# Kernel optimization log

Hardware: AMD Instinct MI355X
Metric: run time of the kernel (lower is better)

The kernel has to match this reference:

```python
import jax, jax.numpy as jnp
import numpy as np

NUM_HEADS = 8
OUT_DIM = 128
DEPTH = OUT_DIM // NUM_HEADS  # 16


def setup_inputs() -> dict:
    key = jax.random.key(0)
    ks = jax.random.split(key, 6)
    B, N, F_IN = 32, 512, 64
    x = jax.random.normal(ks[0], (B, N, F_IN), dtype=jnp.float32)
    adj = jax.random.uniform(ks[1], (B, N, N), dtype=jnp.float32)
    wq = jax.random.normal(ks[2], (F_IN, OUT_DIM), dtype=jnp.float32) * 0.05
    wk = jax.random.normal(ks[3], (F_IN, OUT_DIM), dtype=jnp.float32) * 0.05
    wv = jax.random.normal(ks[4], (F_IN, OUT_DIM), dtype=jnp.float32) * 0.05
    wo = jax.random.normal(ks[5], (OUT_DIM, OUT_DIM), dtype=jnp.float32) * 0.05
    return {"x": x, "adj": adj, "wq": wq, "wk": wk, "wv": wv, "wo": wo}


def _split_heads(t, B, N):
    # [B, N, out_dim] -> [B, H, N, D]
    return t.reshape(B, N, NUM_HEADS, DEPTH).transpose(0, 2, 1, 3)


def reference(x, adj, wq, wk, wv, wo):
    B, N, _ = x.shape
    q = _split_heads(x @ wq, B, N)  # [B,H,N,D]
    k = _split_heads(x @ wk, B, N)
    v = _split_heads(x @ wv, B, N)
    scale = jnp.sqrt(jnp.float32(DEPTH))
    scores = jnp.einsum("bhnd,bhmd->bhnm", q, k) / scale  # [B,H,N,N]
    attn = jnp.tanh(scores * adj[:, None, :, :])  # mask-multiply + tanh
    h = jnp.einsum("bhnm,bhmd->bhnd", attn, v)  # [B,H,N,D]
    h = h.transpose(0, 2, 1, 3).reshape(B, N, OUT_DIM)
    return jax.nn.relu(h @ wo)
```

## Files before the change

kernel.cpp:

```cpp
#include <hip/hip_runtime.h>


typedef __bf16 bf16x8 __attribute__((ext_vector_type(8)));
typedef __bf16 bf16x4 __attribute__((ext_vector_type(4)));
typedef float  f32x4  __attribute__((ext_vector_type(4)));

#define MFMA16(a, b, c) __builtin_amdgcn_mfma_f32_16x16x32_bf16((a), (b), (c), 0, 0, 0)

__global__ __launch_bounds__(256) void prep_kernel(
    const float* __restrict__ wq, const float* __restrict__ wk,
    const float* __restrict__ wv, const float* __restrict__ wo,
    __bf16* __restrict__ WTb, __bf16* __restrict__ WoTb)
{
    int idx = blockIdx.x * 256 + threadIdx.x;
    if (idx < 6144) {
        int j4 = idx % 96, k = idx / 96, j = j4 * 4;
        const float* w = (j < 128) ? wq : ((j < 256) ? wk : wv);
        f32x4 v = *(const f32x4*)&w[k * 128 + (j & 127)];
#pragma unroll
        for (int e = 0; e < 4; ++e) WTb[(j + e) * 64 + k] = (__bf16)v[e];
    } else if (idx < 6144 + 4096) {
        int i2 = idx - 6144;
        int j4 = i2 % 32, k = i2 / 32, j = j4 * 4;
        f32x4 v = *(const f32x4*)&wo[k * 128 + j];
#pragma unroll
        for (int e = 0; e < 4; ++e) WoTb[(j + e) * 128 + k] = (__bf16)v[e];
    }
}

__global__ __launch_bounds__(256) void qkv_kernel(
    const float* __restrict__ x, const __bf16* __restrict__ WTb,
    __bf16* __restrict__ Qb, __bf16* __restrict__ Kb, __bf16* __restrict__ VT)
{
    const int tid = threadIdx.x, lane = tid & 63, w = tid >> 6;
    const int g = lane >> 4, lr = lane & 15;
    const long R0 = (long)blockIdx.x * 16;
    const int b = (int)(R0 >> 9);
    const int nloc = (int)(R0 & 511) + g * 4;

    bf16x8 af[2];
#pragma unroll
    for (int kk = 0; kk < 2; ++kk) {
        const float* xp = x + (R0 + lr) * 64 + kk * 32 + g * 8;
        f32x4 x0 = *(const f32x4*)xp, x1 = *(const f32x4*)(xp + 4);
        bf16x8 a;
#pragma unroll
        for (int e = 0; e < 4; ++e) { a[e] = (__bf16)x0[e]; a[4 + e] = (__bf16)x1[e]; }
        af[kk] = a;
    }

#pragma unroll 2
    for (int i = 0; i < 6; ++i) {
        const int j0 = (w * 6 + i) * 16;
        f32x4 acc = {0.f, 0.f, 0.f, 0.f};
#pragma unroll
        for (int kk = 0; kk < 2; ++kk) {
            bf16x8 bf = *(const bf16x8*)&WTb[(j0 + lr) * 64 + kk * 32 + g * 8];
            acc = MFMA16(af[kk], bf, acc);
        }
        const int jj = (j0 + lr) & 127, hh = jj >> 4, d = jj & 15;
        const int bh = b * 8 + hh, t = j0 >> 7;
        if (t == 2) {
            bf16x4 pk;
#pragma unroll
            for (int r = 0; r < 4; ++r) pk[r] = (__bf16)acc[r];
            *(bf16x4*)&VT[((long)bh * 16 + d) * 512 + nloc] = pk;
        } else {
            __bf16* dst = t ? Kb : Qb;
#pragma unroll
            for (int r = 0; r < 4; ++r)
                dst[((long)bh * 512 + nloc + r) * 16 + d] = (__bf16)acc[r];
        }
    }
}

__device__ __forceinline__ float tanh_e(float x) {
    float e = __builtin_amdgcn_exp2f(x);
    return 1.0f - 2.0f * __builtin_amdgcn_rcpf(e + 1.0f);
}

struct Tile {
    bf16x8 kf0, kf1;
    bf16x4 v0, v1;
};

__device__ __forceinline__ Tile load_tile(
    int m0, bool ga, const __bf16* Kbase, int lr, int g, const __bf16* Vrow)
{
    Tile t;
    t.kf0 = {}; t.kf1 = {};
    if (ga) {
        t.kf0 = *(const bf16x8*)&Kbase[(m0 + lr) * 16 + g * 8];
        t.kf1 = *(const bf16x8*)&Kbase[(m0 + 16 + lr) * 16 + g * 8];
    }
    t.v0 = *(const bf16x4*)&Vrow[m0 + g * 4];
    t.v1 = *(const bf16x4*)&Vrow[m0 + 16 + g * 4];
    return t;
}

__device__ __forceinline__ void compute_tile(
    const Tile& t, int m0, bf16x8 qf0, bf16x8 qf1,
    const __bf16* aR0, const __bf16* aR1, int g,
    f32x4& acc0, f32x4& acc1)
{
    bf16x4 ba00 = *(const bf16x4*)&aR0[m0 + g * 4];
    bf16x4 ba01 = *(const bf16x4*)&aR0[m0 + 16 + g * 4];
    bf16x4 ba10 = *(const bf16x4*)&aR1[m0 + g * 4];
    bf16x4 ba11 = *(const bf16x4*)&aR1[m0 + 16 + g * 4];

    const f32x4 z = {0.f, 0.f, 0.f, 0.f};
    f32x4 s00 = MFMA16(t.kf0, qf0, z);
    f32x4 s01 = MFMA16(t.kf1, qf0, z);
    f32x4 s10 = MFMA16(t.kf0, qf1, z);
    f32x4 s11 = MFMA16(t.kf1, qf1, z);

    bf16x8 p0, p1, vf;
#pragma unroll
    for (int r = 0; r < 4; ++r) {
        p0[r]     = (__bf16)tanh_e(s00[r] * (float)ba00[r]);
        p0[4 + r] = (__bf16)tanh_e(s01[r] * (float)ba01[r]);
        p1[r]     = (__bf16)tanh_e(s10[r] * (float)ba10[r]);
        p1[4 + r] = (__bf16)tanh_e(s11[r] * (float)ba11[r]);
        vf[r]     = t.v0[r];
        vf[4 + r] = t.v1[r];
    }
    acc0 = MFMA16(p0, vf, acc0);
    acc1 = MFMA16(p1, vf, acc1);
}

__global__ __launch_bounds__(512, 4) void attn_kernel(
    const float* __restrict__ adj,
    const __bf16* __restrict__ Qb, const __bf16* __restrict__ Kb,
    const __bf16* __restrict__ VT, const __bf16* __restrict__ WoTb,
    float* __restrict__ out)
{
    __shared__ __align__(16) char smem[33280];

    const int tid  = threadIdx.x;
    const int lane = tid & 63;
    const int h    = tid >> 6;
    const int g    = lane >> 4;
    const int lr   = lane & 15;

    const int l  = blockIdx.x;
    const int q  = l >> 3;
    const int b  = (q >> 4) * 8 + (l & 7);
    const int n0 = (q & 15) * 32;
    const int bh = b * 8 + h;

    const float C = 0.7213475204444817f;
    __bf16* adjL = (__bf16*)smem;
    const float* strip = adj + ((long)b * 512 + n0) * 512;
#pragma unroll
    for (int i = 0; i < 8; ++i) {
        int o = i * 2048 + tid * 4;
        f32x4 v = __builtin_nontemporal_load((const f32x4*)(strip + o));
        int row = o >> 9, col = o & 511;
        bf16x4 w;
#pragma unroll
        for (int e = 0; e < 4; ++e) w[e] = (__bf16)(v[e] * C);
        *(bf16x4*)&adjL[row * 520 + col] = w;
    }

    const bool ga = (g < 2);
    bf16x8 qf0 = {}, qf1 = {};
    if (ga) {
        qf0 = *(const bf16x8*)&Qb[((long)bh * 512 + n0 + lr) * 16 + g * 8];
        qf1 = *(const bf16x8*)&Qb[((long)bh * 512 + n0 + 16 + lr) * 16 + g * 8];
    }
    const __bf16* Kbase = Kb + (long)bh * 512 * 16;
    const __bf16* Vrow  = VT + ((long)bh * 16 + lr) * 512;
    const __bf16* aR0   = adjL + lr * 520;
    const __bf16* aR1   = adjL + (16 + lr) * 520;

    __syncthreads();

    f32x4 acc0 = {0.f, 0.f, 0.f, 0.f}, acc1 = {0.f, 0.f, 0.f, 0.f};

    Tile tA = load_tile(0, ga, Kbase, lr, g, Vrow);
#pragma unroll 1
    for (int t = 0; t < 16; t += 2) {
        Tile tB = load_tile((t + 1) * 32, ga, Kbase, lr, g, Vrow);
        compute_tile(tA, t * 32, qf0, qf1, aR0, aR1, g, acc0, acc1);
        if (t + 2 < 16)
            tA = load_tile((t + 2) * 32, ga, Kbase, lr, g, Vrow);
        compute_tile(tB, (t + 1) * 32, qf0, qf1, aR0, aR1, g, acc0, acc1);
    }

    __syncthreads();
    float* hL = (float*)smem;
#pragma unroll
    for (int r = 0; r < 4; ++r) {
        hL[(g * 4 + r) * 132 + h * 16 + lr]        = acc0[r];
        hL[(16 + g * 4 + r) * 132 + h * 16 + lr]   = acc1[r];
    }
    __syncthreads();

    f32x4 o0 = {0.f, 0.f, 0.f, 0.f}, o1 = {0.f, 0.f, 0.f, 0.f};
#pragma unroll
    for (int kt = 0; kt < 4; ++kt) {
        bf16x8 wf = *(const bf16x8*)&WoTb[(h * 16 + lr) * 128 + kt * 32 + g * 8];
        const float* hp0 = &hL[lr * 132 + kt * 32 + g * 8];
        const float* hp1 = &hL[(16 + lr) * 132 + kt * 32 + g * 8];
        f32x4 ha = *(const f32x4*)hp0, hb = *(const f32x4*)(hp0 + 4);
        f32x4 hc = *(const f32x4*)hp1, hd = *(const f32x4*)(hp1 + 4);
        bf16x8 a0, a1;
#pragma unroll
        for (int e = 0; e < 4; ++e) {
            a0[e] = (__bf16)ha[e]; a0[4 + e] = (__bf16)hb[e];
            a1[e] = (__bf16)hc[e]; a1[4 + e] = (__bf16)hd[e];
        }
        o0 = MFMA16(a0, wf, o0);
        o1 = MFMA16(a1, wf, o1);
    }

    const long obase = (long)b * 512 + n0;
#pragma unroll
    for (int r = 0; r < 4; ++r) {
        out[(obase + g * 4 + r) * 128 + h * 16 + lr]      = fmaxf(o0[r], 0.f);
        out[(obase + 16 + g * 4 + r) * 128 + h * 16 + lr] = fmaxf(o1[r], 0.f);
    }
}

extern "C" void kernel_launch(void* const* d_in, const int* in_sizes, int n_in,
                              void* d_out, int out_size, void* d_ws, size_t ws_size,
                              hipStream_t stream) {
    const float* x   = (const float*)d_in[0];
    const float* adj = (const float*)d_in[1];
    const float* wq  = (const float*)d_in[2];
    const float* wk  = (const float*)d_in[3];
    const float* wv  = (const float*)d_in[4];
    const float* wo  = (const float*)d_in[5];
    float* out = (float*)d_out;

    char* wsb = (char*)d_ws;
    __bf16* WTb  = (__bf16*)wsb;
    __bf16* WoTb = (__bf16*)(wsb + 49152);
    __bf16* Qb   = (__bf16*)(wsb + 81920);
    __bf16* Kb   = Qb + 2097152;
    __bf16* VT   = Kb + 2097152;

    prep_kernel<<<40, 256, 0, stream>>>(wq, wk, wv, wo, WTb, WoTb);
    qkv_kernel<<<1024, 256, 0, stream>>>(x, WTb, Qb, Kb, VT);
    attn_kernel<<<512, 512, 0, stream>>>(adj, Qb, Kb, VT, WoTb, out);
}
```

Baseline: 124.3 us.

## Deepen K/V prefetch to three tiles ahead and raise wave priority around MFMA

The attention inner loop now keeps three K/V tiles in flight instead of one, fully unrolled into a 4-tile rotating schedule with a drained epilogue. This hides more global load latency. It also wraps the compute section in s_setprio(1)/s_setprio(0) so waves doing MFMA/tanh work get issue priority over waves that are loading. The trade is higher register pressure under launch_bounds(512,4), which could cause spills or lower occupancy.

```diff
diff --git a/kernel.cpp b/kernel.cpp
--- a/kernel.cpp
+++ b/kernel.cpp
@@ -108,6 +108,7 @@
     bf16x4 ba10 = *(const bf16x4*)&aR1[m0 + g * 4];
     bf16x4 ba11 = *(const bf16x4*)&aR1[m0 + 16 + g * 4];
 
+    __builtin_amdgcn_s_setprio(1);
     const f32x4 z = {0.f, 0.f, 0.f, 0.f};
     f32x4 s00 = MFMA16(t.kf0, qf0, z);
     f32x4 s01 = MFMA16(t.kf1, qf0, z);
@@ -126,6 +127,7 @@
     }
     acc0 = MFMA16(p0, vf, acc0);
     acc1 = MFMA16(p1, vf, acc1);
+    __builtin_amdgcn_s_setprio(0);
 }
 
 __global__ __launch_bounds__(512, 4) void attn_kernel(
@@ -177,15 +179,27 @@
 
     f32x4 acc0 = {0.f, 0.f, 0.f, 0.f}, acc1 = {0.f, 0.f, 0.f, 0.f};
 
-    Tile tA = load_tile(0, ga, Kbase, lr, g, Vrow);
-#pragma unroll 1
-    for (int t = 0; t < 16; t += 2) {
-        Tile tB = load_tile((t + 1) * 32, ga, Kbase, lr, g, Vrow);
-        compute_tile(tA, t * 32, qf0, qf1, aR0, aR1, g, acc0, acc1);
-        if (t + 2 < 16)
-            tA = load_tile((t + 2) * 32, ga, Kbase, lr, g, Vrow);
-        compute_tile(tB, (t + 1) * 32, qf0, qf1, aR0, aR1, g, acc0, acc1);
-    }
+    Tile T0 = load_tile(0 * 32, ga, Kbase, lr, g, Vrow);
+    Tile T1 = load_tile(1 * 32, ga, Kbase, lr, g, Vrow);
+    Tile T2 = load_tile(2 * 32, ga, Kbase, lr, g, Vrow);
+    Tile T3;
+#pragma unroll
+    for (int j = 0; j < 3; ++j) {
+        const int t = j * 4;
+        T3 = load_tile((t + 3) * 32, ga, Kbase, lr, g, Vrow);
+        compute_tile(T0, t * 32,       qf0, qf1, aR0, aR1, g, acc0, acc1);
+        T0 = load_tile((t + 4) * 32, ga, Kbase, lr, g, Vrow);
+        compute_tile(T1, (t + 1) * 32, qf0, qf1, aR0, aR1, g, acc0, acc1);
+        T1 = load_tile((t + 5) * 32, ga, Kbase, lr, g, Vrow);
+        compute_tile(T2, (t + 2) * 32, qf0, qf1, aR0, aR1, g, acc0, acc1);
+        T2 = load_tile((t + 6) * 32, ga, Kbase, lr, g, Vrow);
+        compute_tile(T3, (t + 3) * 32, qf0, qf1, aR0, aR1, g, acc0, acc1);
+    }
+    T3 = load_tile(15 * 32, ga, Kbase, lr, g, Vrow);
+    compute_tile(T0, 12 * 32, qf0, qf1, aR0, aR1, g, acc0, acc1);
+    compute_tile(T1, 13 * 32, qf0, qf1, aR0, aR1, g, acc0, acc1);
+    compute_tile(T2, 14 * 32, qf0, qf1, aR0, aR1, g, acc0, acc1);
+    compute_tile(T3, 15 * 32, qf0, qf1, aR0, aR1, g, acc0, acc1);
 
     __syncthreads();
     float* hL = (float*)smem;
```

After: 125.3 us. Within noise of the previous version (+0.8%).

## Split attention key range across two wave groups with 1024-thread blocks

Applied to the files above, without the earlier changes.

Doubles the attention block to 16 waves: each head is handled by two waves that each cover half of the 512 keys, and their partial results are reduced through shared memory in two phases. The output projection is also split so each wave computes 16 rows instead of 32. The inner loop is fully unrolled and the MFMA/tanh section is wrapped in s_setprio to favour compute waves. The aim is more waves in flight to hide latency, at the cost of extra LDS reduction, barriers and a register budget that the (1024, 8) launch bounds may tighten.

```diff
diff --git a/kernel.cpp b/kernel.cpp
--- a/kernel.cpp
+++ b/kernel.cpp
@@ -108,6 +108,7 @@
     bf16x4 ba10 = *(const bf16x4*)&aR1[m0 + g * 4];
     bf16x4 ba11 = *(const bf16x4*)&aR1[m0 + 16 + g * 4];
 
+    __builtin_amdgcn_s_setprio(1);
     const f32x4 z = {0.f, 0.f, 0.f, 0.f};
     f32x4 s00 = MFMA16(t.kf0, qf0, z);
     f32x4 s01 = MFMA16(t.kf1, qf0, z);
@@ -126,9 +127,10 @@
     }
     acc0 = MFMA16(p0, vf, acc0);
     acc1 = MFMA16(p1, vf, acc1);
-}
-
-__global__ __launch_bounds__(512, 4) void attn_kernel(
+    __builtin_amdgcn_s_setprio(0);
+}
+
+__global__ __launch_bounds__(1024, 8) void attn_kernel(
     const float* __restrict__ adj,
     const __bf16* __restrict__ Qb, const __bf16* __restrict__ Kb,
     const __bf16* __restrict__ VT, const __bf16* __restrict__ WoTb,
@@ -138,7 +140,9 @@
 
     const int tid  = threadIdx.x;
     const int lane = tid & 63;
-    const int h    = tid >> 6;
+    const int w    = tid >> 6;
+    const int h    = w & 7;
+    const int mh   = w >> 3;
     const int g    = lane >> 4;
     const int lr   = lane & 15;
 
@@ -152,14 +156,14 @@
     __bf16* adjL = (__bf16*)smem;
     const float* strip = adj + ((long)b * 512 + n0) * 512;
 #pragma unroll
-    for (int i = 0; i < 8; ++i) {
-        int o = i * 2048 + tid * 4;
+    for (int i = 0; i < 4; ++i) {
+        int o = i * 4096 + tid * 4;
         f32x4 v = __builtin_nontemporal_load((const f32x4*)(strip + o));
         int row = o >> 9, col = o & 511;
-        bf16x4 w;
-#pragma unroll
-        for (int e = 0; e < 4; ++e) w[e] = (__bf16)(v[e] * C);
-        *(bf16x4*)&adjL[row * 520 + col] = w;
+        bf16x4 wv4;
+#pragma unroll
+        for (int e = 0; e < 4; ++e) wv4[e] = (__bf16)(v[e] * C);
+        *(bf16x4*)&adjL[row * 520 + col] = wv4;
     }
 
     const bool ga = (g < 2);
@@ -177,49 +181,56 @@
 
     f32x4 acc0 = {0.f, 0.f, 0.f, 0.f}, acc1 = {0.f, 0.f, 0.f, 0.f};
 
-    Tile tA = load_tile(0, ga, Kbase, lr, g, Vrow);
-#pragma unroll 1
-    for (int t = 0; t < 16; t += 2) {
-        Tile tB = load_tile((t + 1) * 32, ga, Kbase, lr, g, Vrow);
-        compute_tile(tA, t * 32, qf0, qf1, aR0, aR1, g, acc0, acc1);
-        if (t + 2 < 16)
-            tA = load_tile((t + 2) * 32, ga, Kbase, lr, g, Vrow);
-        compute_tile(tB, (t + 1) * 32, qf0, qf1, aR0, aR1, g, acc0, acc1);
+    const int mbase = mh * 256;
+    Tile tA = load_tile(mbase, ga, Kbase, lr, g, Vrow);
+#pragma unroll
+    for (int t = 0; t < 8; t += 2) {
+        Tile tB = load_tile(mbase + (t + 1) * 32, ga, Kbase, lr, g, Vrow);
+        compute_tile(tA, mbase + t * 32, qf0, qf1, aR0, aR1, g, acc0, acc1);
+        if (t + 2 < 8)
+            tA = load_tile(mbase + (t + 2) * 32, ga, Kbase, lr, g, Vrow);
+        compute_tile(tB, mbase + (t + 1) * 32, qf0, qf1, aR0, aR1, g, acc0, acc1);
     }
 
     __syncthreads();
     float* hL = (float*)smem;
-#pragma unroll
-    for (int r = 0; r < 4; ++r) {
-        hL[(g * 4 + r) * 132 + h * 16 + lr]        = acc0[r];
-        hL[(16 + g * 4 + r) * 132 + h * 16 + lr]   = acc1[r];
-    }
-    __syncthreads();
-
-    f32x4 o0 = {0.f, 0.f, 0.f, 0.f}, o1 = {0.f, 0.f, 0.f, 0.f};
+    const int c0 = (g * 4) * 132 + h * 16 + lr;
+    const int c1 = (16 + g * 4) * 132 + h * 16 + lr;
+    if (mh == 0) {
+#pragma unroll
+        for (int r = 0; r < 4; ++r) {
+            hL[c0 + r * 132] = acc0[r];
+            hL[c1 + r * 132] = acc1[r];
+        }
+    }
+    __syncthreads();
+    if (mh == 1) {
+#pragma unroll
+        for (int r = 0; r < 4; ++r) {
+            hL[c0 + r * 132] += acc0[r];
+            hL[c1 + r * 132] += acc1[r];
+        }
+    }
+    __syncthreads();
+
+    const int ns = mh;
+    const int j0 = h * 16;
+    f32x4 o0 = {0.f, 0.f, 0.f, 0.f};
 #pragma unroll
     for (int kt = 0; kt < 4; ++kt) {
-        bf16x8 wf = *(const bf16x8*)&WoTb[(h * 16 + lr) * 128 + kt * 32 + g * 8];
-        const float* hp0 = &hL[lr * 132 + kt * 32 + g * 8];
-        const float* hp1 = &hL[(16 + lr) * 132 + kt * 32 + g * 8];
-        f32x4 ha = *(const f32x4*)hp0, hb = *(const f32x4*)(hp0 + 4);
-        f32x4 hc = *(const f32x4*)hp1, hd = *(const f32x4*)(hp1 + 4);
-        bf16x8 a0, a1;
-#pragma unroll
-        for (int e = 0; e < 4; ++e) {
-            a0[e] = (__bf16)ha[e]; a0[4 + e] = (__bf16)hb[e];
-            a1[e] = (__bf16)hc[e]; a1[4 + e] = (__bf16)hd[e];
-        }
+        bf16x8 wf = *(const bf16x8*)&WoTb[(j0 + lr) * 128 + kt * 32 + g * 8];
+        const float* hp = &hL[(ns * 16 + lr) * 132 + kt * 32 + g * 8];
+        f32x4 ha = *(const f32x4*)hp, hb = *(const f32x4*)(hp + 4);
+        bf16x8 a0;
+#pragma unroll
+        for (int e = 0; e < 4; ++e) { a0[e] = (__bf16)ha[e]; a0[4 + e] = (__bf16)hb[e]; }
         o0 = MFMA16(a0, wf, o0);
-        o1 = MFMA16(a1, wf, o1);
-    }
-
-    const long obase = (long)b * 512 + n0;
-#pragma unroll
-    for (int r = 0; r < 4; ++r) {
-        out[(obase + g * 4 + r) * 128 + h * 16 + lr]      = fmaxf(o0[r], 0.f);
-        out[(obase + 16 + g * 4 + r) * 128 + h * 16 + lr] = fmaxf(o1[r], 0.f);
-    }
+    }
+
+    const long obase = (long)b * 512 + n0 + ns * 16;
+#pragma unroll
+    for (int r = 0; r < 4; ++r)
+        out[(obase + g * 4 + r) * 128 + j0 + lr] = fmaxf(o0[r], 0.f);
 }
 
 extern "C" void kernel_launch(void* const* d_in, const int* in_sizes, int n_in,
@@ -242,5 +253,5 @@
 
     prep_kernel<<<40, 256, 0, stream>>>(wq, wk, wv, wo, WTb, WoTb);
     qkv_kernel<<<1024, 256, 0, stream>>>(x, WTb, Qb, Kb, VT);
-    attn_kernel<<<512, 512, 0, stream>>>(adj, Qb, Kb, VT, WoTb, out);
-}
+    attn_kernel<<<512, 1024, 0, stream>>>(adj, Qb, Kb, VT, WoTb, out);
+}
```

Result: slower. 139.4 us (+12.1%).
